# Kernel tuning notes

Measured on AMD Instinct MI355X. Metric: run time of the kernel, lower is better.

Reference implementation:

```python
import jax, jax.numpy as jnp
import numpy as np

B, T, D, H = 32, 1024, 512, 256  # batch, seq_len, input_size, lstm hidden per direction (2H == D)


def _lstm_dir(x_tbd, W_ih, W_hh, b):
    """Single-direction LSTM over time-major input [T, B, D] -> hidden states [T, B, H].
    PyTorch gate order: i, f, g, o."""
    xg = jnp.einsum('tbd,gd->tbg', x_tbd, W_ih) + b  # precompute input projections [T,B,4H]
    h0 = jnp.zeros((x_tbd.shape[1], W_hh.shape[1]), x_tbd.dtype)

    def step(carry, xt):
        h, c = carry
        g = xt + h @ W_hh.T
        i, f, gg, o = jnp.split(g, 4, axis=-1)
        c = jax.nn.sigmoid(f) * c + jax.nn.sigmoid(i) * jnp.tanh(gg)
        h = jax.nn.sigmoid(o) * jnp.tanh(c)
        return (h, c), h

    _, hs = jax.lax.scan(step, (h0, h0), xg)
    return hs


def setup_inputs() -> dict:
    key = jax.random.key(0)
    ks = jax.random.split(key, 10)
    s = 0.05
    # padding mask: 1 (True) for padding positions, built from random valid lengths
    lengths = jax.random.randint(ks[1], (B,), T // 2, T)
    x_mask = jnp.arange(T)[None, :] >= lengths[:, None]  # bool [B, T]
    return {
        'x': jax.random.normal(ks[0], (B, T, D), jnp.float32),
        'x_mask': x_mask,
        'W_ih_f': jax.random.normal(ks[2], (4 * H, D), jnp.float32) * s,
        'W_hh_f': jax.random.normal(ks[3], (4 * H, H), jnp.float32) * s,
        'b_f': jnp.zeros((4 * H,), jnp.float32),
        'W_ih_b': jax.random.normal(ks[4], (4 * H, D), jnp.float32) * s,
        'W_hh_b': jax.random.normal(ks[5], (4 * H, H), jnp.float32) * s,
        'b_b': jnp.zeros((4 * H,), jnp.float32),
        'W_l': jax.random.normal(ks[6], (D, D), jnp.float32) * s,
    }


def reference(x, x_mask, W_ih_f, W_hh_f, b_f, W_ih_b, W_hh_b, b_b, W_l):
    # BiRNN encode: 1-layer bidirectional LSTM, concat directions -> [B, T, 2H] == [B, T, D]
    xt = jnp.swapaxes(x, 0, 1)  # [T, B, D]
    h_f = _lstm_dir(xt, W_ih_f, W_hh_f, b_f)
    h_b = _lstm_dir(xt[::-1], W_ih_b, W_hh_b, b_b)[::-1]
    xe = jnp.swapaxes(jnp.concatenate([h_f, h_b], axis=-1), 0, 1)  # [B, T, D]

    # Bilinear self-attention: L = (x W_l^T) x^T, mask padded query rows, softmax, weighted sum
    proj = xe @ W_l.T  # [B, T, D]
    L = jnp.einsum('bid,bjd->bij', proj, xe)  # [B, T, T]
    L = jnp.where(x_mask[:, :, None], jnp.float32(-1e30), L)
    A = jax.nn.softmax(L, axis=-1)
    return jnp.einsum('bij,bjd->bid', A, xe)  # [B, T, D]
```

## Files before the change

### kernel.cpp

```cpp
#include <hip/hip_runtime.h>
#include <math.h>

#define T_SEQ 1024
#define B_SZ  32
#define D_SZ  512
#define H_SZ  256

typedef unsigned short u16;
typedef short v8bf __attribute__((ext_vector_type(8)));
typedef float v4f  __attribute__((ext_vector_type(4)));

__device__ __forceinline__ unsigned int f2bf(float f)
{
    unsigned int u = __float_as_uint(f);
    return (u + 0x7fffu + ((u >> 16) & 1u)) >> 16;
}
__device__ __forceinline__ u16 f2bfu(float f)
{
    unsigned int u = __float_as_uint(f);
    return (u16)((u + 0x7fffu + ((u >> 16) & 1u)) >> 16);
}
__device__ __forceinline__ float bfu2f(u16 h)
{
    return __uint_as_float(((unsigned int)h) << 16);
}

__device__ __forceinline__ void gload_lds16(const void* g, void* l)
{
    __builtin_amdgcn_global_load_lds(
        (const __attribute__((address_space(1))) void*)g,
        (__attribute__((address_space(3))) void*)l,
        16, 0, 0);
}

__device__ __forceinline__ float tanh_fast(float x)
{
    float xc = fminf(fmaxf(x, -30.f), 30.f);
    float e = __expf(-2.f * xc);
    return (1.f - e) / (1.f + e);
}

#define BM 64
#define BN 64
#define BK 16

__global__ __launch_bounds__(256)
void gemm_nt(const float* __restrict__ A, const float* __restrict__ W,
             const float* __restrict__ bias, float* __restrict__ C,
             int M, int N, int K,
             long long sA, long long sW, long long sC)
{
    int z = blockIdx.z;
    A += (size_t)z * sA; W += (size_t)z * sW; C += (size_t)z * sC;
    int n0 = blockIdx.x * BN;
    int m0 = blockIdx.y * BM;
    int tid = threadIdx.x;
    int tm = tid >> 4, tn = tid & 15;

    __shared__ float As[BK][BM + 4];
    __shared__ float Ws[BK][BN + 4];

    float acc[4][4] = {};

    int lc = tid & 15;
    int lr = tid >> 4;

    for (int k0 = 0; k0 < K; k0 += BK) {
        #pragma unroll
        for (int i = 0; i < 4; ++i) {
            int r = lr + 16 * i;
            As[lc][r] = A[(size_t)(m0 + r) * K + k0 + lc];
            Ws[lc][r] = W[(size_t)(n0 + r) * K + k0 + lc];
        }
        __syncthreads();
        #pragma unroll
        for (int kk = 0; kk < BK; ++kk) {
            float4 a4 = *(const float4*)&As[kk][tm * 4];
            float4 b4 = *(const float4*)&Ws[kk][tn * 4];
            float a[4] = {a4.x, a4.y, a4.z, a4.w};
            float b[4] = {b4.x, b4.y, b4.z, b4.w};
            #pragma unroll
            for (int i = 0; i < 4; ++i)
                #pragma unroll
                for (int j = 0; j < 4; ++j)
                    acc[i][j] = fmaf(a[i], b[j], acc[i][j]);
        }
        __syncthreads();
    }

    float bb[4] = {0.f, 0.f, 0.f, 0.f};
    if (bias) {
        #pragma unroll
        for (int j = 0; j < 4; ++j) bb[j] = bias[n0 + tn * 4 + j];
    }
    #pragma unroll
    for (int i = 0; i < 4; ++i) {
        int m = m0 + tm * 4 + i;
        float4 o;
        o.x = acc[i][0] + bb[0];
        o.y = acc[i][1] + bb[1];
        o.z = acc[i][2] + bb[2];
        o.w = acc[i][3] + bb[3];
        *(float4*)&C[(size_t)m * N + n0 + tn * 4] = o;
    }
}

__global__ __launch_bounds__(256)
void gemm_nn(const float* __restrict__ A, const float* __restrict__ B,
             float* __restrict__ C, int M, int N, int K,
             long long sA, long long sB, long long sC)
{
    int z = blockIdx.z;
    A += (size_t)z * sA; B += (size_t)z * sB; C += (size_t)z * sC;
    int n0 = blockIdx.x * BN;
    int m0 = blockIdx.y * BM;
    int tid = threadIdx.x;
    int tm = tid >> 4, tn = tid & 15;

    __shared__ float As[BK][BM + 4];
    __shared__ float Bs[BK][BN + 4];

    float acc[4][4] = {};

    int lc = tid & 15;
    int lr = tid >> 4;
    int br = tid >> 6;
    int bc = tid & 63;

    for (int k0 = 0; k0 < K; k0 += BK) {
        #pragma unroll
        for (int i = 0; i < 4; ++i) {
            int r = lr + 16 * i;
            As[lc][r] = A[(size_t)(m0 + r) * K + k0 + lc];
        }
        #pragma unroll
        for (int i = 0; i < 4; ++i) {
            int r = br + 4 * i;
            Bs[r][bc] = B[(size_t)(k0 + r) * N + n0 + bc];
        }
        __syncthreads();
        #pragma unroll
        for (int kk = 0; kk < BK; ++kk) {
            float4 a4 = *(const float4*)&As[kk][tm * 4];
            float4 b4 = *(const float4*)&Bs[kk][tn * 4];
            float a[4] = {a4.x, a4.y, a4.z, a4.w};
            float b[4] = {b4.x, b4.y, b4.z, b4.w};
            #pragma unroll
            for (int i = 0; i < 4; ++i)
                #pragma unroll
                for (int j = 0; j < 4; ++j)
                    acc[i][j] = fmaf(a[i], b[j], acc[i][j]);
        }
        __syncthreads();
    }
    #pragma unroll
    for (int i = 0; i < 4; ++i) {
        int m = m0 + tm * 4 + i;
        float4 o;
        o.x = acc[i][0]; o.y = acc[i][1]; o.z = acc[i][2]; o.w = acc[i][3];
        *(float4*)&C[(size_t)m * N + n0 + tn * 4] = o;
    }
}

template<int EPI>
__global__ __launch_bounds__(256)
void gemm_ms(const u16* __restrict__ Ah, const u16* __restrict__ Al,
             const u16* __restrict__ Bh, const u16* __restrict__ Bl,
             const float* __restrict__ bias,
             float* __restrict__ C, u16* __restrict__ Chi, u16* __restrict__ Clo,
             int M, int N, int K,
             long long sA, long long sB, long long sC)
{
    int z = blockIdx.z;
    Ah += (size_t)z * sA; Al += (size_t)z * sA;
    Bh += (size_t)z * sB; Bl += (size_t)z * sB;
    int n0 = blockIdx.x * 128;
    int m0 = blockIdx.y * 128;
    int t  = threadIdx.x;
    int lane = t & 63, wid = t >> 6;

    __shared__ u16 sA_h[128 * 32];
    __shared__ u16 sA_l[128 * 32];
    __shared__ u16 sB_h[128 * 32];
    __shared__ u16 sB_l[128 * 32];

    int wm = (wid & 1) << 6;
    int wn = (wid >> 1) << 6;
    int fr = lane & 15;
    int g  = lane >> 4;

    v4f acc[4][4];
    #pragma unroll
    for (int i = 0; i < 4; ++i)
        #pragma unroll
        for (int j = 0; j < 4; ++j)
            acc[i][j] = (v4f){0.f, 0.f, 0.f, 0.f};

    int s0 = t;
    int s1 = t + 256;
    int r0 = s0 >> 2, gl0 = (s0 & 3) ^ ((s0 >> 3) & 3);
    int r1 = s1 >> 2, gl1 = (s1 & 3) ^ ((s1 >> 3) & 3);
    int lb0 = (wid << 6) << 3;
    int lb1 = ((wid << 6) + 256) << 3;

    for (int k0 = 0; k0 < K; k0 += 32) {
        size_t gA0 = (size_t)(m0 + r0) * K + k0 + gl0 * 8;
        size_t gA1 = (size_t)(m0 + r1) * K + k0 + gl1 * 8;
        size_t gB0 = (size_t)(n0 + r0) * K + k0 + gl0 * 8;
        size_t gB1 = (size_t)(n0 + r1) * K + k0 + gl1 * 8;
        gload_lds16(Ah + gA0, sA_h + lb0);
        gload_lds16(Ah + gA1, sA_h + lb1);
        gload_lds16(Al + gA0, sA_l + lb0);
        gload_lds16(Al + gA1, sA_l + lb1);
        gload_lds16(Bh + gB0, sB_h + lb0);
        gload_lds16(Bh + gB1, sB_h + lb1);
        gload_lds16(Bl + gB0, sB_l + lb0);
        gload_lds16(Bl + gB1, sB_l + lb1);
        __syncthreads();

        #pragma unroll
        for (int pass = 0; pass < 3; ++pass) {
            const u16* sB_p = (pass == 2) ? sB_l : sB_h;
            const u16* sA_p = (pass == 1) ? sA_l : sA_h;
            v8bf bf[4];
            #pragma unroll
            for (int ni = 0; ni < 4; ++ni) {
                int r = wn + ni * 16 + fr;
                bf[ni] = *(const v8bf*)&sB_p[r * 32 + ((g ^ ((r >> 1) & 3)) << 3)];
            }
            #pragma unroll
            for (int mi = 0; mi < 4; ++mi) {
                int r = wm + mi * 16 + fr;
                v8bf af = *(const v8bf*)&sA_p[r * 32 + ((g ^ ((r >> 1) & 3)) << 3)];
                #pragma unroll
                for (int ni = 0; ni < 4; ++ni)
                    acc[mi][ni] = __builtin_amdgcn_mfma_f32_16x16x32_bf16(
                        af, bf[ni], acc[mi][ni], 0, 0, 0);
            }
        }
        __syncthreads();
    }

    int ocol = lane & 15;
    int orow = (lane >> 4) << 2;
    if (EPI == 1) {
        #pragma unroll
        for (int mi = 0; mi < 4; ++mi) {
            #pragma unroll
            for (int rr = 0; rr < 4; ++rr) {
                int m = m0 + wm + mi * 16 + orow + rr;
                #pragma unroll
                for (int ni = 0; ni < 4; ++ni) {
                    int n = n0 + wn + ni * 16 + ocol;
                    float v = acc[mi][ni][rr];
                    u16 h = f2bfu(v);
                    Chi[(size_t)m * N + n] = h;
                    Clo[(size_t)m * N + n] = f2bfu(v - bfu2f(h));
                }
            }
        }
    } else {
        float* Cz = C + (size_t)z * sC;
        float bb[4] = {0.f, 0.f, 0.f, 0.f};
        if (bias) {
            #pragma unroll
            for (int ni = 0; ni < 4; ++ni) bb[ni] = bias[n0 + wn + ni * 16 + ocol];
        }
        #pragma unroll
        for (int mi = 0; mi < 4; ++mi) {
            #pragma unroll
            for (int rr = 0; rr < 4; ++rr) {
                int m = m0 + wm + mi * 16 + orow + rr;
                #pragma unroll
                for (int ni = 0; ni < 4; ++ni) {
                    int n = n0 + wn + ni * 16 + ocol;
                    Cz[(size_t)m * N + n] = acc[mi][ni][rr] + bb[ni];
                }
            }
        }
    }
}

__global__ __launch_bounds__(256)
void convert_split(const float4* __restrict__ in,
                   ushort4* __restrict__ hi, ushort4* __restrict__ lo)
{
    size_t i = (size_t)blockIdx.x * 256 + threadIdx.x;
    float4 v = in[i];
    ushort4 h, l;
    h.x = f2bfu(v.x); l.x = f2bfu(v.x - bfu2f(h.x));
    h.y = f2bfu(v.y); l.y = f2bfu(v.y - bfu2f(h.y));
    h.z = f2bfu(v.z); l.z = f2bfu(v.z - bfu2f(h.z));
    h.w = f2bfu(v.w); l.w = f2bfu(v.w - bfu2f(h.w));
    hi[i] = h;
    lo[i] = l;
}

__global__ __launch_bounds__(256)
void transpose_split_xe(const float* __restrict__ xe,
                        u16* __restrict__ Th, u16* __restrict__ Tl)
{
    int b = blockIdx.z;
    const float* X = xe + (size_t)b * T_SEQ * D_SZ;
    u16* TH = Th + (size_t)b * T_SEQ * D_SZ;
    u16* TL = Tl + (size_t)b * T_SEQ * D_SZ;
    int t0 = blockIdx.x << 5, d0 = blockIdx.y << 5;

    __shared__ float tile[32][33];
    int tx = threadIdx.x & 31, ty = threadIdx.x >> 5;

    #pragma unroll
    for (int i = 0; i < 4; ++i)
        tile[ty + (i << 3)][tx] = X[(size_t)(t0 + ty + (i << 3)) * D_SZ + d0 + tx];
    __syncthreads();
    #pragma unroll
    for (int i = 0; i < 4; ++i) {
        int dd = ty + (i << 3);
        float v = tile[tx][dd];
        u16 h = f2bfu(v);
        TH[(size_t)(d0 + dd) * T_SEQ + t0 + tx] = h;
        TL[(size_t)(d0 + dd) * T_SEQ + t0 + tx] = f2bfu(v - bfu2f(h));
    }
}

__global__ __launch_bounds__(256)
void pack_whh_bf16(const float* __restrict__ Wf, const float* __restrict__ Wb,
                   uint4* __restrict__ Wpf, uint4* __restrict__ Wpb)
{
    int idx = blockIdx.x * 256 + threadIdx.x;
    int u = idx & (H_SZ - 1);
    int p = idx >> 8;
    uint4 a, b;
    unsigned int* pa = (unsigned int*)&a;
    unsigned int* pb = (unsigned int*)&b;
    #pragma unroll
    for (int g = 0; g < 4; ++g) {
        size_t row = (size_t)(g * H_SZ + u) * H_SZ;
        pa[g] = f2bf(Wf[row + 2 * p]) | (f2bf(Wf[row + 2 * p + 1]) << 16);
        pb[g] = f2bf(Wb[row + 2 * p]) | (f2bf(Wb[row + 2 * p + 1]) << 16);
    }
    Wpf[idx] = a;
    Wpb[idx] = b;
}

__global__ __launch_bounds__(256)
void pack_w_rows(const float4* __restrict__ Wf, const float4* __restrict__ Wb,
                 ushort4* __restrict__ Of, ushort4* __restrict__ Ob)
{
    size_t i = (size_t)blockIdx.x * 256 + threadIdx.x;
    float4 a = Wf[i], b = Wb[i];
    ushort4 oa, ob;
    oa.x = f2bfu(a.x); oa.y = f2bfu(a.y); oa.z = f2bfu(a.z); oa.w = f2bfu(a.w);
    ob.x = f2bfu(b.x); ob.y = f2bfu(b.y); ob.z = f2bfu(b.z); ob.w = f2bfu(b.w);
    Of[i] = oa;
    Ob[i] = ob;
}

__global__ __launch_bounds__(512, 2)
void lstm_mfma(const float* __restrict__ xgA, const u16* __restrict__ WA,
               const float* __restrict__ xgB, const u16* __restrict__ WB,
               float* __restrict__ xe)
{
    int bi  = blockIdx.x;
    int dir = bi >> 1;
    int b0  = (bi & 1) * 16;
    const float* xg = dir ? xgB : xgA;
    const u16*  W   = dir ? WB : WA;

    int tid  = threadIdx.x;
    int lane = tid & 63, wv = tid >> 6;
    int wn   = wv << 7;
    int fr   = lane & 15;
    int kg   = lane >> 4;

    __shared__ u16  hHi[16 * 256];
    __shared__ u16  hLo[16 * 256];
    __shared__ float gate[16][1024 + 4];

    for (int i = tid; i < 16 * 256; i += 512) { hHi[i] = 0; hLo[i] = 0; }

    const u16* bp[8];
    #pragma unroll
    for (int ni = 0; ni < 8; ++ni)
        bp[ni] = W + (size_t)(wn + ni * 16 + fr) * 256 + kg * 8;

    int u  = tid & 255;
    int bh = tid >> 8;
    float c8[8];
    #pragma unroll
    for (int j = 0; j < 8; ++j) c8[j] = 0.f;

    __syncthreads();

    for (int s = 0; s < T_SEQ; ++s) {
        int t = dir ? (T_SEQ - 1 - s) : s;

        float pxi[8], pxf[8], pxg[8], pxo[8];
        #pragma unroll
        for (int j = 0; j < 8; ++j) {
            int bl = bh * 8 + j;
            const float* row = xg + ((size_t)(b0 + bl) * T_SEQ + t) * (4 * H_SZ);
            pxi[j] = row[u];
            pxf[j] = row[256 + u];
            pxg[j] = row[512 + u];
            pxo[j] = row[768 + u];
        }

        v4f accH[8], accL[8];
        #pragma unroll
        for (int ni = 0; ni < 8; ++ni) {
            accH[ni] = (v4f){0.f, 0.f, 0.f, 0.f};
            accL[ni] = (v4f){0.f, 0.f, 0.f, 0.f};
        }

        #pragma unroll
        for (int ks = 0; ks < 8; ++ks) {
            int aoff = fr * 512 + ((((ks << 2) + kg) ^ (fr & 7)) << 4);
            v8bf aH = *(const v8bf*)((const char*)hHi + aoff);
            v8bf aL = *(const v8bf*)((const char*)hLo + aoff);
            #pragma unroll
            for (int ni = 0; ni < 8; ++ni) {
                v8bf bf = *(const v8bf*)(bp[ni] + ks * 32);
                accH[ni] = __builtin_amdgcn_mfma_f32_16x16x32_bf16(aH, bf, accH[ni], 0, 0, 0);
                accL[ni] = __builtin_amdgcn_mfma_f32_16x16x32_bf16(aL, bf, accL[ni], 0, 0, 0);
            }
        }

        int orow = kg << 2;
        #pragma unroll
        for (int ni = 0; ni < 8; ++ni) {
            #pragma unroll
            for (int r = 0; r < 4; ++r)
                gate[orow + r][wn + ni * 16 + fr] = accH[ni][r] + accL[ni][r];
        }
        __syncthreads();

        #pragma unroll
        for (int j = 0; j < 8; ++j) {
            int bl = bh * 8 + j;
            float ai = pxi[j] + gate[bl][u];
            float af = pxf[j] + gate[bl][256 + u];
            float ag = pxg[j] + gate[bl][512 + u];
            float ao = pxo[j] + gate[bl][768 + u];
            float ig = 1.f / (1.f + __expf(-ai));
            float fg = 1.f / (1.f + __expf(-af));
            float gv = tanh_fast(ag);
            float og = 1.f / (1.f + __expf(-ao));
            c8[j] = fg * c8[j] + ig * gv;
            float hv = og * tanh_fast(c8[j]);
            xe[((size_t)(b0 + bl) * T_SEQ + t) * D_SZ + dir * H_SZ + u] = hv;
            u16 hh = f2bfu(hv);
            u16 hl = f2bfu(hv - bfu2f(hh));
            int hoff = bl * 512 + ((((u >> 3) ^ (bl & 7)) << 4)) + ((u & 7) << 1);
            *(u16*)((char*)hHi + hoff) = hh;
            *(u16*)((char*)hLo + hoff) = hl;
        }
        __syncthreads();
    }
}

__global__ __launch_bounds__(1024)
void lstm_bf16(const float* __restrict__ xgA, const uint4* __restrict__ WpA,
               const float* __restrict__ xgB, const uint4* __restrict__ WpB,
               float* __restrict__ xe, int d0, int fused)
{
    int i = blockIdx.x;
    int b, dir;
    if (fused) {
        int j = i & 7, m = i >> 3;
        dir = j >> 2;
        b   = (j & 3) * 8 + m;
    } else {
        b   = (i & 3) * 8 + (i >> 2);
        dir = d0;
    }
    const float* xg = dir ? xgB : xgA;
    const uint4* Wp = dir ? WpB : WpA;

    int tid   = threadIdx.x;
    int u     = tid & (H_SZ - 1);
    int slice = tid >> 8;
    int p0    = slice << 5;

    __shared__ float  hs[H_SZ];
    __shared__ float4 part[4][H_SZ];

    uint4 wres[16];
    {
        const uint4* wb = Wp + (size_t)p0 * H_SZ + u;
        #pragma unroll
        for (int q = 0; q < 16; ++q) wres[q] = wb[q * H_SZ];
    }
    const uint4* wstream = Wp + (size_t)(p0 + 16) * H_SZ + u;

    if (tid < H_SZ) hs[tid] = 0.f;
    float c = 0.f;
    __syncthreads();

    for (int s = 0; s < T_SEQ; ++s) {
        int t = dir ? (T_SEQ - 1 - s) : s;

        float xi = 0.f, xf = 0.f, xgv = 0.f, xo = 0.f;
        if (tid < H_SZ) {
            const float* row = xg + ((size_t)b * T_SEQ + t) * (4 * H_SZ);
            xi  = row[u];
            xf  = row[H_SZ + u];
            xgv = row[2 * H_SZ + u];
            xo  = row[3 * H_SZ + u];
        }

        float4 acc; acc.x = 0.f; acc.y = 0.f; acc.z = 0.f; acc.w = 0.f;

        #define DOT_PAIR(WQ, P)                                             \
        {                                                                   \
            float2 hp = *(const float2*)&hs[2 * (P)];                       \
            const unsigned int* wc = (const unsigned int*)&(WQ);            \
            _Pragma("unroll")                                               \
            for (int g = 0; g < 4; ++g) {                                   \
                float wlo = __uint_as_float(wc[g] << 16);                   \
                float whi = __uint_as_float(wc[g] & 0xffff0000u);           \
                ((float*)&acc)[g] =                                         \
                    fmaf(whi, hp.y, fmaf(wlo, hp.x, ((float*)&acc)[g]));    \
            }                                                               \
        }

        #pragma unroll
        for (int q = 0; q < 16; ++q) {
            DOT_PAIR(wres[q], p0 + q);
        }
        #pragma unroll
        for (int q = 0; q < 16; ++q) {
            int qr = (q + s) & 15;
            uint4 wq = wstream[(size_t)qr * H_SZ];
            DOT_PAIR(wq, p0 + 16 + qr);
        }
        #undef DOT_PAIR

        part[slice][u] = acc;
        __syncthreads();

        if (tid < H_SZ) {
            float4 pp0 = part[0][u], pp1 = part[1][u], pp2 = part[2][u], pp3 = part[3][u];
            float ai = xi  + pp0.x + pp1.x + pp2.x + pp3.x;
            float af = xf  + pp0.y + pp1.y + pp2.y + pp3.y;
            float ag = xgv + pp0.z + pp1.z + pp2.z + pp3.z;
            float ao = xo  + pp0.w + pp1.w + pp2.w + pp3.w;
            float ig = 1.f / (1.f + __expf(-ai));
            float fg = 1.f / (1.f + __expf(-af));
            float gg = tanh_fast(ag);
            float og = 1.f / (1.f + __expf(-ao));
            c = fg * c + ig * gg;
            float h = og * tanh_fast(c);
            hs[u] = h;
            xe[((size_t)b * T_SEQ + t) * D_SZ + dir * H_SZ + u] = h;
        }
        __syncthreads();
    }
}

__global__ __launch_bounds__(256)
void softmax_rows(float* __restrict__ L, const void* __restrict__ maskraw)
{
    const unsigned char* mu8 = (const unsigned char*)maskraw;
    const int*           mi32 = (const int*)maskraw;
    bool layout_u8 = (mu8[1023] != 0);

    int lane = threadIdx.x & 63;
    int wid  = threadIdx.x >> 6;
    int row  = (blockIdx.x << 2) + wid;
    float* p = L + (size_t)row * T_SEQ;

    int mval = layout_u8 ? (int)mu8[row] : mi32[row];

    if (mval != 0) {
        const float inv = 1.0f / (float)T_SEQ;
        for (int j = lane; j < T_SEQ; j += 64) p[j] = inv;
        return;
    }

    float v[16];
    float m = -1e30f;
    #pragma unroll
    for (int u = 0; u < 16; ++u) {
        v[u] = p[lane + (u << 6)];
        m = fmaxf(m, v[u]);
    }
    #pragma unroll
    for (int s = 32; s; s >>= 1) m = fmaxf(m, __shfl_xor(m, s, 64));

    float sum = 0.f;
    #pragma unroll
    for (int u = 0; u < 16; ++u) {
        v[u] = __expf(v[u] - m);
        sum += v[u];
    }
    #pragma unroll
    for (int s = 32; s; s >>= 1) sum += __shfl_xor(sum, s, 64);

    float inv = 1.0f / sum;
    #pragma unroll
    for (int u = 0; u < 16; ++u) p[lane + (u << 6)] = v[u] * inv;
}

extern "C" void kernel_launch(void* const* d_in, const int* in_sizes, int n_in,
                              void* d_out, int out_size, void* d_ws, size_t ws_size,
                              hipStream_t stream)
{
    const float* x     = (const float*)d_in[0];
    const void*  xmask = d_in[1];
    const float* Wih_f = (const float*)d_in[2];
    const float* Whh_f = (const float*)d_in[3];
    const float* b_f   = (const float*)d_in[4];
    const float* Wih_b = (const float*)d_in[5];
    const float* Whh_b = (const float*)d_in[6];
    const float* b_b   = (const float*)d_in[7];
    const float* W_l   = (const float*)d_in[8];
    float* out = (float*)d_out;

    char* ws = (char*)d_ws;
    const size_t MB1 = (size_t)1 << 20;
    const size_t SZ_XE = (size_t)B_SZ * T_SEQ * D_SZ * sizeof(float);
    const size_t SZ_XG = (size_t)B_SZ * T_SEQ * 4 * H_SZ * sizeof(float);
    bool fused = ws_size >= SZ_XE + 2 * SZ_XG;

    const int MT = B_SZ * T_SEQ;
    const long long sTD = (long long)T_SEQ * D_SZ;
    const long long sTT = (long long)T_SEQ * T_SEQ;

    if (fused) {
        u16* x_hi  = (u16*)(ws);
        u16* x_lo  = (u16*)(ws + 32 * MB1);
        float* xg_f = (float*)(ws + 64 * MB1);
        float* xg_b = (float*)(ws + 192 * MB1);
        float* xe   = (float*)(ws);
        u16* xe_hi = (u16*)(ws + 64 * MB1);
        u16* xe_lo = (u16*)(ws + 96 * MB1);
        u16* pj_hi = (u16*)(ws + 128 * MB1);
        u16* pj_lo = (u16*)(ws + 160 * MB1);
        float* L   = (float*)(ws + 192 * MB1);
        u16* xT_hi = pj_hi;
        u16* xT_lo = pj_lo;
        u16* L_hi  = (u16*)(ws);
        u16* L_lo  = (u16*)(ws + 64 * MB1);

        u16* WB_f    = (u16*)d_out;
        u16* WB_b    = (u16*)((char*)d_out + (MB1 >> 1));
        u16* Wihf_hi = (u16*)((char*)d_out + 1 * MB1);
        u16* Wihf_lo = (u16*)((char*)d_out + 2 * MB1);
        u16* Wihb_hi = (u16*)((char*)d_out + 3 * MB1);
        u16* Wihb_lo = (u16*)((char*)d_out + 4 * MB1);
        u16* Wl_hi   = (u16*)((char*)d_out + 5 * MB1);
        u16* Wl_lo   = (u16*)((char*)d_out + 5 * MB1 + (MB1 >> 1));

        pack_w_rows<<<dim3((4 * H_SZ * H_SZ) / 1024), dim3(256), 0, stream>>>(
            (const float4*)Whh_f, (const float4*)Whh_b,
            (ushort4*)WB_f, (ushort4*)WB_b);
        convert_split<<<dim3((MT * D_SZ) / 1024), dim3(256), 0, stream>>>(
            (const float4*)x, (ushort4*)x_hi, (ushort4*)x_lo);
        convert_split<<<dim3((4 * H_SZ * D_SZ) / 1024), dim3(256), 0, stream>>>(
            (const float4*)Wih_f, (ushort4*)Wihf_hi, (ushort4*)Wihf_lo);
        convert_split<<<dim3((4 * H_SZ * D_SZ) / 1024), dim3(256), 0, stream>>>(
            (const float4*)Wih_b, (ushort4*)Wihb_hi, (ushort4*)Wihb_lo);
        convert_split<<<dim3((D_SZ * D_SZ) / 1024), dim3(256), 0, stream>>>(
            (const float4*)W_l, (ushort4*)Wl_hi, (ushort4*)Wl_lo);

        gemm_ms<0><<<dim3((4 * H_SZ) / 128, MT / 128, 1), dim3(256), 0, stream>>>(
            x_hi, x_lo, Wihf_hi, Wihf_lo, b_f, xg_f, nullptr, nullptr,
            MT, 4 * H_SZ, D_SZ, 0, 0, 0);
        gemm_ms<0><<<dim3((4 * H_SZ) / 128, MT / 128, 1), dim3(256), 0, stream>>>(
            x_hi, x_lo, Wihb_hi, Wihb_lo, b_b, xg_b, nullptr, nullptr,
            MT, 4 * H_SZ, D_SZ, 0, 0, 0);

        lstm_mfma<<<dim3(4), dim3(512), 0, stream>>>(
            xg_f, WB_f, xg_b, WB_b, xe);

        convert_split<<<dim3((MT * D_SZ) / 1024), dim3(256), 0, stream>>>(
            (const float4*)xe, (ushort4*)xe_hi, (ushort4*)xe_lo);

        gemm_ms<1><<<dim3(D_SZ / 128, MT / 128, 1), dim3(256), 0, stream>>>(
            xe_hi, xe_lo, Wl_hi, Wl_lo, nullptr, nullptr, pj_hi, pj_lo,
            MT, D_SZ, D_SZ, 0, 0, 0);

        gemm_ms<0><<<dim3(T_SEQ / 128, T_SEQ / 128, B_SZ), dim3(256), 0, stream>>>(
            pj_hi, pj_lo, xe_hi, xe_lo, nullptr, L, nullptr, nullptr,
            T_SEQ, T_SEQ, D_SZ, sTD, sTD, sTT);

        softmax_rows<<<dim3(MT / 4), dim3(256), 0, stream>>>(L, xmask);

        transpose_split_xe<<<dim3(T_SEQ / 32, D_SZ / 32, B_SZ), dim3(256), 0, stream>>>(
            xe, xT_hi, xT_lo);

        convert_split<<<dim3((MT * T_SEQ) / 1024), dim3(256), 0, stream>>>(
            (const float4*)L, (ushort4*)L_hi, (ushort4*)L_lo);

        gemm_ms<0><<<dim3(D_SZ / 128, T_SEQ / 128, B_SZ), dim3(256), 0, stream>>>(
            L_hi, L_lo, xT_hi, xT_lo, nullptr, out, nullptr, nullptr,
            T_SEQ, D_SZ, T_SEQ, sTT, sTD, sTD);
    } else {
        uint4* Wpf = (uint4*)d_out;
        uint4* Wpb = (uint4*)d_out + 128 * H_SZ;
        float* xe   = (float*)(ws);
        float* xg_f = (float*)(ws + SZ_XE);
        float* xg_b = xg_f;
        float* L    = xg_f;
        float* proj = out;

        pack_whh_bf16<<<dim3((128 * H_SZ) / 256), dim3(256), 0, stream>>>(
            Whh_f, Whh_b, Wpf, Wpb);
        gemm_nt<<<dim3((4 * H_SZ) / BN, MT / BM, 1), dim3(256), 0, stream>>>(
            x, Wih_f, b_f, xg_f, MT, 4 * H_SZ, D_SZ, 0, 0, 0);
        lstm_bf16<<<dim3(B_SZ), dim3(1024), 0, stream>>>(
            xg_f, Wpf, xg_f, Wpf, xe, 0, 0);
        gemm_nt<<<dim3((4 * H_SZ) / BN, MT / BM, 1), dim3(256), 0, stream>>>(
            x, Wih_b, b_b, xg_b, MT, 4 * H_SZ, D_SZ, 0, 0, 0);
        lstm_bf16<<<dim3(B_SZ), dim3(1024), 0, stream>>>(
            xg_b, Wpb, xg_b, Wpb, xe, 1, 0);

        gemm_nt<<<dim3(D_SZ / BN, MT / BM, 1), dim3(256), 0, stream>>>(
            xe, W_l, nullptr, proj, MT, D_SZ, D_SZ, 0, 0, 0);
        gemm_nt<<<dim3(T_SEQ / BN, T_SEQ / BM, B_SZ), dim3(256), 0, stream>>>(
            proj, xe, nullptr, L, T_SEQ, T_SEQ, D_SZ, sTD, sTD, sTT);
        softmax_rows<<<dim3(MT / 4), dim3(256), 0, stream>>>(L, xmask);
        gemm_nn<<<dim3(D_SZ / BN, T_SEQ / BM, B_SZ), dim3(256), 0, stream>>>(
            L, xe, out, T_SEQ, D_SZ, T_SEQ, sTT, sTD, sTD);
    }
}
```

Baseline: 17.00 ms.

## Chunk LSTM input projection and attention to shrink workspace for the fused path

Restructures the fused MFMA path so it needs about 192 MB of workspace instead of xe plus two full gate buffers. The input projection is computed in 256-step time chunks. The LSTM kernel saves and restores h/c state between chunk launches. Attention (projection, scores, softmax, weighted sum) runs over four groups of 8 batches, reusing a smaller L buffer. The transpose now reuses the already-split xe hi/lo planes instead of re-splitting floats. This likely lets the faster bf16-split MFMA path run where the fallback path ran before, at the cost of many more kernel launches and serialized chunk boundaries.

```diff
diff --git a/kernel.cpp b/kernel.cpp
--- a/kernel.cpp
+++ b/kernel.cpp
@@ -297,29 +297,33 @@
 }
 
 __global__ __launch_bounds__(256)
-void transpose_split_xe(const float* __restrict__ xe,
-                        u16* __restrict__ Th, u16* __restrict__ Tl)
+void transpose_pair(const u16* __restrict__ Sh, const u16* __restrict__ Sl,
+                    u16* __restrict__ Th, u16* __restrict__ Tl)
 {
     int b = blockIdx.z;
-    const float* X = xe + (size_t)b * T_SEQ * D_SZ;
+    const u16* XH = Sh + (size_t)b * T_SEQ * D_SZ;
+    const u16* XL = Sl + (size_t)b * T_SEQ * D_SZ;
     u16* TH = Th + (size_t)b * T_SEQ * D_SZ;
     u16* TL = Tl + (size_t)b * T_SEQ * D_SZ;
     int t0 = blockIdx.x << 5, d0 = blockIdx.y << 5;
 
-    __shared__ float tile[32][33];
+    __shared__ unsigned int tile[32][33];
     int tx = threadIdx.x & 31, ty = threadIdx.x >> 5;
 
     #pragma unroll
-    for (int i = 0; i < 4; ++i)
-        tile[ty + (i << 3)][tx] = X[(size_t)(t0 + ty + (i << 3)) * D_SZ + d0 + tx];
+    for (int i = 0; i < 4; ++i) {
+        int tt = ty + (i << 3);
+        size_t off = (size_t)(t0 + tt) * D_SZ + d0 + tx;
+        tile[tt][tx] = (unsigned int)XH[off] | ((unsigned int)XL[off] << 16);
+    }
     __syncthreads();
     #pragma unroll
     for (int i = 0; i < 4; ++i) {
         int dd = ty + (i << 3);
-        float v = tile[tx][dd];
-        u16 h = f2bfu(v);
-        TH[(size_t)(d0 + dd) * T_SEQ + t0 + tx] = h;
-        TL[(size_t)(d0 + dd) * T_SEQ + t0 + tx] = f2bfu(v - bfu2f(h));
+        unsigned int v = tile[tx][dd];
+        size_t off = (size_t)(d0 + dd) * T_SEQ + t0 + tx;
+        TH[off] = (u16)(v & 0xffffu);
+        TL[off] = (u16)(v >> 16);
     }
 }
 
@@ -357,15 +361,16 @@
 }
 
 __global__ __launch_bounds__(512, 2)
-void lstm_mfma(const float* __restrict__ xgA, const u16* __restrict__ WA,
+void lstm_mfma(const float* __restrict__ xgF, const u16* __restrict__ WF,
                const float* __restrict__ xgB, const u16* __restrict__ WB,
-               float* __restrict__ xe)
+               float* __restrict__ xe, float* __restrict__ stH,
+               float* __restrict__ stC, int chunk)
 {
     int bi  = blockIdx.x;
     int dir = bi >> 1;
     int b0  = (bi & 1) * 16;
-    const float* xg = dir ? xgB : xgA;
-    const u16*  W   = dir ? WB : WA;
+    const float* xg = dir ? xgB : xgF;
+    const u16*  W   = dir ? WB : WF;
 
     int tid  = threadIdx.x;
     int lane = tid & 63, wv = tid >> 6;
@@ -377,8 +382,6 @@
     __shared__ u16  hLo[16 * 256];
     __shared__ float gate[16][1024 + 4];
 
-    for (int i = tid; i < 16 * 256; i += 512) { hHi[i] = 0; hLo[i] = 0; }
-
     const u16* bp[8];
     #pragma unroll
     for (int ni = 0; ni < 8; ++ni)
@@ -386,20 +389,34 @@
 
     int u  = tid & 255;
     int bh = tid >> 8;
-    float c8[8];
-    #pragma unroll
-    for (int j = 0; j < 8; ++j) c8[j] = 0.f;
-
+    float c8[8], hv8[8];
+    #pragma unroll
+    for (int j = 0; j < 8; ++j) {
+        int bl = bh * 8 + j;
+        float hv = 0.f, cv = 0.f;
+        if (chunk != 0) {
+            size_t si = (size_t)dir * 8192 + (size_t)(b0 + bl) * 256 + u;
+            hv = stH[si];
+            cv = stC[si];
+        }
+        c8[j] = cv; hv8[j] = hv;
+        u16 hh = f2bfu(hv);
+        u16 hl = f2bfu(hv - bfu2f(hh));
+        int hoff = bl * 512 + (((u >> 3) ^ (bl & 7)) << 4) + ((u & 7) << 1);
+        *(u16*)((char*)hHi + hoff) = hh;
+        *(u16*)((char*)hLo + hoff) = hl;
+    }
     __syncthreads();
 
-    for (int s = 0; s < T_SEQ; ++s) {
-        int t = dir ? (T_SEQ - 1 - s) : s;
+    for (int sl = 0; sl < 256; ++sl) {
+        int tc = dir ? (255 - sl) : sl;
+        int t  = dir ? (1023 - 256 * chunk - sl) : (256 * chunk + sl);
 
         float pxi[8], pxf[8], pxg[8], pxo[8];
         #pragma unroll
         for (int j = 0; j < 8; ++j) {
             int bl = bh * 8 + j;
-            const float* row = xg + ((size_t)(b0 + bl) * T_SEQ + t) * (4 * H_SZ);
+            const float* row = xg + ((size_t)(b0 + bl) * 256 + tc) * 1024;
             pxi[j] = row[u];
             pxf[j] = row[256 + u];
             pxg[j] = row[512 + u];
@@ -448,14 +465,23 @@
             float og = 1.f / (1.f + __expf(-ao));
             c8[j] = fg * c8[j] + ig * gv;
             float hv = og * tanh_fast(c8[j]);
+            hv8[j] = hv;
             xe[((size_t)(b0 + bl) * T_SEQ + t) * D_SZ + dir * H_SZ + u] = hv;
             u16 hh = f2bfu(hv);
             u16 hl = f2bfu(hv - bfu2f(hh));
-            int hoff = bl * 512 + ((((u >> 3) ^ (bl & 7)) << 4)) + ((u & 7) << 1);
+            int hoff = bl * 512 + (((u >> 3) ^ (bl & 7)) << 4) + ((u & 7) << 1);
             *(u16*)((char*)hHi + hoff) = hh;
             *(u16*)((char*)hLo + hoff) = hl;
         }
         __syncthreads();
+    }
+
+    #pragma unroll
+    for (int j = 0; j < 8; ++j) {
+        int bl = bh * 8 + j;
+        size_t si = (size_t)dir * 8192 + (size_t)(b0 + bl) * 256 + u;
+        stH[si] = hv8[j];
+        stC[si] = c8[j];
     }
 }
 
@@ -559,7 +585,8 @@
 }
 
 __global__ __launch_bounds__(256)
-void softmax_rows(float* __restrict__ L, const void* __restrict__ maskraw)
+void softmax_rows(float* __restrict__ L, const void* __restrict__ maskraw,
+                  int row0)
 {
     const unsigned char* mu8 = (const unsigned char*)maskraw;
     const int*           mi32 = (const int*)maskraw;
@@ -570,7 +597,8 @@
     int row  = (blockIdx.x << 2) + wid;
     float* p = L + (size_t)row * T_SEQ;
 
-    int mval = layout_u8 ? (int)mu8[row] : mi32[row];
+    int grow = row0 + row;
+    int mval = layout_u8 ? (int)mu8[grow] : mi32[grow];
 
     if (mval != 0) {
         const float inv = 1.0f / (float)T_SEQ;
@@ -621,42 +649,44 @@
     const size_t MB1 = (size_t)1 << 20;
     const size_t SZ_XE = (size_t)B_SZ * T_SEQ * D_SZ * sizeof(float);
     const size_t SZ_XG = (size_t)B_SZ * T_SEQ * 4 * H_SZ * sizeof(float);
-    bool fused = ws_size >= SZ_XE + 2 * SZ_XG;
+    bool fused = ws_size >= 192 * MB1;
 
     const int MT = B_SZ * T_SEQ;
     const long long sTD = (long long)T_SEQ * D_SZ;
     const long long sTT = (long long)T_SEQ * T_SEQ;
 
     if (fused) {
-        u16* x_hi  = (u16*)(ws);
-        u16* x_lo  = (u16*)(ws + 32 * MB1);
+        u16*  x_hi  = (u16*)(ws);
+        u16*  x_lo  = (u16*)(ws + 32 * MB1);
         float* xg_f = (float*)(ws + 64 * MB1);
-        float* xg_b = (float*)(ws + 192 * MB1);
-        float* xe   = (float*)(ws);
-        u16* xe_hi = (u16*)(ws + 64 * MB1);
-        u16* xe_lo = (u16*)(ws + 96 * MB1);
-        u16* pj_hi = (u16*)(ws + 128 * MB1);
-        u16* pj_lo = (u16*)(ws + 160 * MB1);
-        float* L   = (float*)(ws + 192 * MB1);
-        u16* xT_hi = pj_hi;
-        u16* xT_lo = pj_lo;
-        u16* L_hi  = (u16*)(ws);
-        u16* L_lo  = (u16*)(ws + 64 * MB1);
-
-        u16* WB_f    = (u16*)d_out;
-        u16* WB_b    = (u16*)((char*)d_out + (MB1 >> 1));
+        float* xg_b = (float*)(ws + 96 * MB1);
+        float* xe   = (float*)(ws + 128 * MB1);
+        u16*  xe_hi = (u16*)(ws);
+        u16*  xe_lo = (u16*)(ws + 32 * MB1);
+        u16*  xT_hi = (u16*)(ws + 64 * MB1);
+        u16*  xT_lo = (u16*)(ws + 96 * MB1);
+        u16*  pj_hi = (u16*)(ws + 128 * MB1);
+        u16*  pj_lo = (u16*)(ws + 136 * MB1);
+        float* L    = (float*)(ws + 144 * MB1);
+        u16*  L_hi  = (u16*)(ws + 176 * MB1);
+        u16*  L_lo  = (u16*)(ws + 128 * MB1);
+
         u16* Wihf_hi = (u16*)((char*)d_out + 1 * MB1);
         u16* Wihf_lo = (u16*)((char*)d_out + 2 * MB1);
         u16* Wihb_hi = (u16*)((char*)d_out + 3 * MB1);
         u16* Wihb_lo = (u16*)((char*)d_out + 4 * MB1);
-        u16* Wl_hi   = (u16*)((char*)d_out + 5 * MB1);
-        u16* Wl_lo   = (u16*)((char*)d_out + 5 * MB1 + (MB1 >> 1));
-
+        u16* WB_f    = (u16*)((char*)d_out + 60 * MB1);
+        u16* WB_b    = (u16*)((char*)d_out + 60 * MB1 + (MB1 >> 1));
+        float* stH   = (float*)((char*)d_out + 61 * MB1);
+        float* stC   = (float*)((char*)d_out + 61 * MB1 + 65536);
+        u16* Wl_hi   = (u16*)((char*)d_out + 63 * MB1);
+        u16* Wl_lo   = (u16*)((char*)d_out + 63 * MB1 + (MB1 >> 1));
+
+        convert_split<<<dim3((MT * D_SZ) / 1024), dim3(256), 0, stream>>>(
+            (const float4*)x, (ushort4*)x_hi, (ushort4*)x_lo);
         pack_w_rows<<<dim3((4 * H_SZ * H_SZ) / 1024), dim3(256), 0, stream>>>(
             (const float4*)Whh_f, (const float4*)Whh_b,
             (ushort4*)WB_f, (ushort4*)WB_b);
-        convert_split<<<dim3((MT * D_SZ) / 1024), dim3(256), 0, stream>>>(
-            (const float4*)x, (ushort4*)x_hi, (ushort4*)x_lo);
         convert_split<<<dim3((4 * H_SZ * D_SZ) / 1024), dim3(256), 0, stream>>>(
             (const float4*)Wih_f, (ushort4*)Wihf_hi, (ushort4*)Wihf_lo);
         convert_split<<<dim3((4 * H_SZ * D_SZ) / 1024), dim3(256), 0, stream>>>(
@@ -664,38 +694,42 @@
         convert_split<<<dim3((D_SZ * D_SZ) / 1024), dim3(256), 0, stream>>>(
             (const float4*)W_l, (ushort4*)Wl_hi, (ushort4*)Wl_lo);
 
-        gemm_ms<0><<<dim3((4 * H_SZ) / 128, MT / 128, 1), dim3(256), 0, stream>>>(
-            x_hi, x_lo, Wihf_hi, Wihf_lo, b_f, xg_f, nullptr, nullptr,
-            MT, 4 * H_SZ, D_SZ, 0, 0, 0);
-        gemm_ms<0><<<dim3((4 * H_SZ) / 128, MT / 128, 1), dim3(256), 0, stream>>>(
-            x_hi, x_lo, Wihb_hi, Wihb_lo, b_b, xg_b, nullptr, nullptr,
-            MT, 4 * H_SZ, D_SZ, 0, 0, 0);
-
-        lstm_mfma<<<dim3(4), dim3(512), 0, stream>>>(
-            xg_f, WB_f, xg_b, WB_b, xe);
+        for (int c = 0; c < 4; ++c) {
+            int tbF = 256 * c;
+            int tbB = 768 - 256 * c;
+            gemm_ms<0><<<dim3(8, 2, B_SZ), dim3(256), 0, stream>>>(
+                x_hi + (size_t)tbF * D_SZ, x_lo + (size_t)tbF * D_SZ,
+                Wihf_hi, Wihf_lo, b_f, xg_f, nullptr, nullptr,
+                256, 4 * H_SZ, D_SZ, sTD, 0, 256LL * 1024);
+            gemm_ms<0><<<dim3(8, 2, B_SZ), dim3(256), 0, stream>>>(
+                x_hi + (size_t)tbB * D_SZ, x_lo + (size_t)tbB * D_SZ,
+                Wihb_hi, Wihb_lo, b_b, xg_b, nullptr, nullptr,
+                256, 4 * H_SZ, D_SZ, sTD, 0, 256LL * 1024);
+            lstm_mfma<<<dim3(4), dim3(512), 0, stream>>>(
+                xg_f, WB_f, xg_b, WB_b, xe, stH, stC, c);
+        }
 
         convert_split<<<dim3((MT * D_SZ) / 1024), dim3(256), 0, stream>>>(
             (const float4*)xe, (ushort4*)xe_hi, (ushort4*)xe_lo);
-
-        gemm_ms<1><<<dim3(D_SZ / 128, MT / 128, 1), dim3(256), 0, stream>>>(
-            xe_hi, xe_lo, Wl_hi, Wl_lo, nullptr, nullptr, pj_hi, pj_lo,
-            MT, D_SZ, D_SZ, 0, 0, 0);
-
-        gemm_ms<0><<<dim3(T_SEQ / 128, T_SEQ / 128, B_SZ), dim3(256), 0, stream>>>(
-            pj_hi, pj_lo, xe_hi, xe_lo, nullptr, L, nullptr, nullptr,
-            T_SEQ, T_SEQ, D_SZ, sTD, sTD, sTT);
-
-        softmax_rows<<<dim3(MT / 4), dim3(256), 0, stream>>>(L, xmask);
-
-        transpose_split_xe<<<dim3(T_SEQ / 32, D_SZ / 32, B_SZ), dim3(256), 0, stream>>>(
-            xe, xT_hi, xT_lo);
-
-        convert_split<<<dim3((MT * T_SEQ) / 1024), dim3(256), 0, stream>>>(
-            (const float4*)L, (ushort4*)L_hi, (ushort4*)L_lo);
-
-        gemm_ms<0><<<dim3(D_SZ / 128, T_SEQ / 128, B_SZ), dim3(256), 0, stream>>>(
-            L_hi, L_lo, xT_hi, xT_lo, nullptr, out, nullptr, nullptr,
-            T_SEQ, D_SZ, T_SEQ, sTT, sTD, sTD);
+        transpose_pair<<<dim3(T_SEQ / 32, D_SZ / 32, B_SZ), dim3(256), 0, stream>>>(
+            xe_hi, xe_lo, xT_hi, xT_lo);
+
+        for (int q = 0; q < 4; ++q) {
+            size_t boff = (size_t)q * 8 * sTD;
+            gemm_ms<1><<<dim3(D_SZ / 128, (8 * T_SEQ) / 128, 1), dim3(256), 0, stream>>>(
+                xe_hi + boff, xe_lo + boff, Wl_hi, Wl_lo, nullptr,
+                nullptr, pj_hi, pj_lo, 8 * T_SEQ, D_SZ, D_SZ, 0, 0, 0);
+            gemm_ms<0><<<dim3(T_SEQ / 128, T_SEQ / 128, 8), dim3(256), 0, stream>>>(
+                pj_hi, pj_lo, xe_hi + boff, xe_lo + boff, nullptr,
+                L, nullptr, nullptr, T_SEQ, T_SEQ, D_SZ, sTD, sTD, sTT);
+            softmax_rows<<<dim3((8 * T_SEQ) / 4), dim3(256), 0, stream>>>(
+                L, xmask, q * 8 * T_SEQ);
+            convert_split<<<dim3((8 * T_SEQ * T_SEQ) / 1024), dim3(256), 0, stream>>>(
+                (const float4*)L, (ushort4*)L_hi, (ushort4*)L_lo);
+            gemm_ms<0><<<dim3(D_SZ / 128, T_SEQ / 128, 8), dim3(256), 0, stream>>>(
+                L_hi, L_lo, xT_hi + boff, xT_lo + boff, nullptr,
+                out + boff, nullptr, nullptr, T_SEQ, D_SZ, T_SEQ, sTT, sTD, sTD);
+        }
     } else {
         uint4* Wpf = (uint4*)d_out;
         uint4* Wpb = (uint4*)d_out + 128 * H_SZ;
@@ -720,7 +754,7 @@
             xe, W_l, nullptr, proj, MT, D_SZ, D_SZ, 0, 0, 0);
         gemm_nt<<<dim3(T_SEQ / BN, T_SEQ / BM, B_SZ), dim3(256), 0, stream>>>(
             proj, xe, nullptr, L, T_SEQ, T_SEQ, D_SZ, sTD, sTD, sTT);
-        softmax_rows<<<dim3(MT / 4), dim3(256), 0, stream>>>(L, xmask);
+        softmax_rows<<<dim3(MT / 4), dim3(256), 0, stream>>>(L, xmask, 0);
         gemm_nn<<<dim3(D_SZ / BN, T_SEQ / BM, B_SZ), dim3(256), 0, stream>>>(
             L, xe, out, T_SEQ, D_SZ, T_SEQ, sTT, sTD, sTD);
     }
```

After: 13.77 ms. -19.0%, faster.
